# Performance work log

Hardware: AMD Instinct MI355X
Metric: run time of the kernel (lower is better)

The kernel has to match this reference:

```python
import jax, jax.numpy as jnp
import numpy as np

D_MODEL = 512
N_HEADS = 8
HEAD_DIM = D_MODEL // N_HEADS
B, L, S = 4, 2048, 2048


def setup_inputs() -> dict:
    key = jax.random.key(0)
    ks = jax.random.split(key, 16)
    std = 1.0 / np.sqrt(D_MODEL)
    inp = {
        'queries': jax.random.normal(ks[0], (B, L, D_MODEL), jnp.float32),
        'keys': jax.random.normal(ks[1], (B, S, D_MODEL), jnp.float32),
        'values': jax.random.normal(ks[2], (B, S, D_MODEL), jnp.float32),
        'tau': jax.random.uniform(ks[3], (B,), jnp.float32, 0.5, 1.5),
        'delta': jax.random.normal(ks[4], (B,), jnp.float32) * 0.1,
        'Wq': jax.random.normal(ks[5], (D_MODEL, D_MODEL), jnp.float32) * std,
        'bq': jnp.zeros((D_MODEL,), jnp.float32),
        'Wk': jax.random.normal(ks[6], (D_MODEL, D_MODEL), jnp.float32) * std,
        'bk': jnp.zeros((D_MODEL,), jnp.float32),
        'Wv': jax.random.normal(ks[7], (D_MODEL, D_MODEL), jnp.float32) * std,
        'bv': jnp.zeros((D_MODEL,), jnp.float32),
        'Wo': jax.random.normal(ks[8], (D_MODEL, D_MODEL), jnp.float32) * std,
        'bo': jnp.zeros((D_MODEL,), jnp.float32),
    }
    return inp


def reference(queries, keys, values, tau, delta, Wq, bq, Wk, bk, Wv, bv, Wo, bo):
    Bq, Lq, _ = queries.shape
    Sk = keys.shape[1]
    H, E = N_HEADS, HEAD_DIM
    # projections -> [B, L, H, E]
    q = (queries @ Wq + bq).reshape(Bq, Lq, H, E)
    k = (keys @ Wk + bk).reshape(Bq, Sk, H, E)
    v = (values @ Wv + bv).reshape(Bq, Sk, H, E)
    scale = 1.0 / jnp.sqrt(jnp.float32(E))
    # scores: [B, H, L, S]
    scores = jnp.einsum('blhe,bshe->bhls', q, k)
    scores = scores * tau[:, None, None, None] + delta[:, None, None, None]
    A = jax.nn.softmax(scale * scores, axis=-1)  # dropout is identity in eval
    out = jnp.einsum('bhls,bshd->blhd', A, v).reshape(Bq, Lq, H * E)
    return out @ Wo + bo
```

## Files before the change

kernel.cpp:

```cpp
#include <hip/hip_runtime.h>
#include <stdint.h>

#define NB 4
#define LQ 2048
#define DM 512
#define NH 8
#define EH 64
#define MT (NB*LQ)
#define QBLK 128

typedef __attribute__((ext_vector_type(4)))  float f32x4;
typedef __attribute__((ext_vector_type(8)))  __bf16 bf16x8;
typedef __attribute__((ext_vector_type(8)))  unsigned short u16x8;
typedef __attribute__((ext_vector_type(4)))  short s16x4;
typedef __attribute__((ext_vector_type(4)))  float float4_t;
typedef __attribute__((ext_vector_type(2)))  unsigned int u32x2;
typedef __attribute__((ext_vector_type(4)))  unsigned int u32x4;

static __device__ __forceinline__ unsigned short f2bf(float f) {
  unsigned int u = __builtin_bit_cast(unsigned int, f);
  u += 0x7fffu + ((u >> 16) & 1u);
  return (unsigned short)(u >> 16);
}

static __device__ __forceinline__ float bf2f(unsigned short h) {
  unsigned int u = ((unsigned int)h) << 16;
  return __builtin_bit_cast(float, u);
}

static __device__ __forceinline__ void gload16(const void* g, void* l) {
  __builtin_amdgcn_global_load_lds(
      (__attribute__((address_space(1))) unsigned int*)(g),
      (__attribute__((address_space(3))) unsigned int*)(l), 16, 0, 0);
}

static __device__ __forceinline__ unsigned int cvt_pk_bf16(float lo, float hi) {
  unsigned int r;
  asm("v_cvt_pk_bf16_f32 %0, %1, %2" : "=v"(r) : "v"(lo), "v"(hi));
  return r;
}

static __device__ __forceinline__ f32x4 mfma16(s16x4 a, s16x4 b, f32x4 c) {
#if defined(__HIP_DEVICE_COMPILE__)
#if __has_builtin(__builtin_amdgcn_mfma_f32_16x16x16bf16_1k)
  return __builtin_amdgcn_mfma_f32_16x16x16bf16_1k(a, b, c, 0, 0, 0);
#else
  f32x4 d;
  asm volatile("v_mfma_f32_16x16x16_bf16 %0, %1, %2, %3"
               : "=v"(d) : "v"(a), "v"(b), "0"(c));
  return d;
#endif
#else
  (void)a; (void)b;
  return c;
#endif
}

extern "C" __global__ __launch_bounds__(256) void k_cast_wt(
    const float* __restrict__ wq, const float* __restrict__ wk,
    const float* __restrict__ wv, const float* __restrict__ wo,
    unsigned short* __restrict__ wt) {
  __shared__ float tile[64][65];
  int z = blockIdx.z;
  const float* w = (z==0)?wq : (z==1)?wk : (z==2)?wv : wo;
  unsigned short* dst = wt + (size_t)z * DM * DM;
  int kb = blockIdx.y * 64, nb = blockIdx.x * 64;
  int t = threadIdx.x;
  int r = t >> 2, c0 = (t & 3) * 16;
  #pragma unroll
  for (int i = 0; i < 16; i += 4) {
    float4_t v4 = *(const float4_t*)(w + (size_t)(kb + r) * DM + nb + c0 + i);
    tile[r][c0+i]   = v4[0]; tile[r][c0+i+1] = v4[1];
    tile[r][c0+i+2] = v4[2]; tile[r][c0+i+3] = v4[3];
  }
  __syncthreads();
  u16x8 o0, o1;
  #pragma unroll
  for (int i = 0; i < 8; ++i) o0[i] = f2bf(tile[c0+i][r]);
  #pragma unroll
  for (int i = 0; i < 8; ++i) o1[i] = f2bf(tile[c0+8+i][r]);
  *(u16x8*)(dst + (size_t)(nb + r) * DM + kb + c0)     = o0;
  *(u16x8*)(dst + (size_t)(nb + r) * DM + kb + c0 + 8) = o1;
}

extern "C" __global__ __launch_bounds__(256) void k_gemm_qkv(
    const float* __restrict__ qin, const float* __restrict__ kin,
    const float* __restrict__ vin, const unsigned short* __restrict__ WT,
    const float* __restrict__ bq, const float* __restrict__ bk,
    const float* __restrict__ bv, const float* __restrict__ tau,
    unsigned short* __restrict__ out) {
  int bid = blockIdx.x;
  int wgid = (bid & 7) * 96 + (bid >> 3);
  int n0 = (wgid & 3) * 128;
  int p = wgid >> 2;
  int z = p % 3;
  int m0 = (p / 3) * 128;

  const float* Af = (z==0)?qin : (z==1)?kin : vin;
  const unsigned short* Bt = WT + (size_t)z * DM * DM;
  const float* bias = (z==0)?bq : (z==1)?bk : bv;
  unsigned short* dst = out + (size_t)z * MT * DM;

  __shared__ unsigned short As[2][128][32];
  __shared__ unsigned short Bs[2][128][32];

  float qsc = (z == 0) ? tau[m0 >> 11] * 0.18033688011112042f : 1.0f;
  int t = threadIdx.x;
  int lane = t & 63;
  int w = t >> 6;
  int wr = w >> 1, wc = w & 1;
  int g = lane >> 4, r15 = lane & 15;

  int ar = t >> 1, ah = t & 1;
  int as = (ar >> 1) & 3;
  int dlo = ((ah*2)     ^ as) * 8;
  int dhi = ((ah*2 + 1) ^ as) * 8;

  float4_t a0, a1, a2, a3;
  auto loadA = [&](int kt) {
    const float* src = Af + (size_t)(m0 + ar)*DM + kt*32 + ah*16;
    a0 = *(const float4_t*)(src);
    a1 = *(const float4_t*)(src + 4);
    a2 = *(const float4_t*)(src + 8);
    a3 = *(const float4_t*)(src + 12);
  };
  auto writeA = [&](int bb) {
    u32x4 lo, hi;
    lo[0] = cvt_pk_bf16(a0[0], a0[1]); lo[1] = cvt_pk_bf16(a0[2], a0[3]);
    lo[2] = cvt_pk_bf16(a1[0], a1[1]); lo[3] = cvt_pk_bf16(a1[2], a1[3]);
    hi[0] = cvt_pk_bf16(a2[0], a2[1]); hi[1] = cvt_pk_bf16(a2[2], a2[3]);
    hi[2] = cvt_pk_bf16(a3[0], a3[1]); hi[3] = cvt_pk_bf16(a3[2], a3[3]);
    *(u32x4*)(&As[bb][ar][dlo]) = lo;
    *(u32x4*)(&As[bb][ar][dhi]) = hi;
  };
  auto stageB = [&](int bb, int kt) {
    int k0 = kt * 32;
    int sblk = (t & 3) ^ ((t >> 3) & 3);
    #pragma unroll
    for (int j=0;j<2;j++) {
      int o = t*16 + j*4096;
      int row = o >> 6;
      gload16(Bt + (size_t)(n0+row)*DM + k0 + sblk*8, (char*)(&Bs[bb][0][0]) + o);
    }
  };

  f32x4 acc[4][4];
  #pragma unroll
  for (int i=0;i<4;i++)
    #pragma unroll
    for (int j=0;j<4;j++)
      #pragma unroll
      for (int e=0;e<4;e++) acc[i][j][e] = 0.f;

  loadA(0);
  writeA(0);
  stageB(0, 0);
  __syncthreads();
  int buf = 0;
  for (int kt = 0; kt < DM/32; ++kt) {
    bool pre = (kt + 1 < DM/32);
    if (pre) { loadA(kt + 1); stageB(buf ^ 1, kt + 1); }
    bf16x8 af[4], bfr[4];
    #pragma unroll
    for (int mi=0;mi<4;mi++) {
      int row = wr*64 + mi*16 + r15;
      int blk = g ^ ((row >> 1) & 3);
      af[mi] = *(const bf16x8*)(&As[buf][row][blk*8]);
    }
    #pragma unroll
    for (int ni=0;ni<4;ni++) {
      int row = wc*64 + ni*16 + r15;
      int blk = g ^ ((row >> 1) & 3);
      bfr[ni] = *(const bf16x8*)(&Bs[buf][row][blk*8]);
    }
    #pragma unroll
    for (int mi=0;mi<4;mi++)
      #pragma unroll
      for (int ni=0;ni<4;ni++)
        acc[mi][ni] = __builtin_amdgcn_mfma_f32_16x16x32_bf16(af[mi], bfr[ni], acc[mi][ni], 0, 0, 0);
    if (pre) writeA(buf ^ 1);
    __syncthreads();
    buf ^= 1;
  }
  #pragma unroll
  for (int ni=0;ni<4;ni++) {
    int n = n0 + wc*64 + ni*16 + r15;
    float bia = bias[n];
    int h = n >> 6, e = n & 63;
    #pragma unroll
    for (int mi=0;mi<4;mi++) {
      #pragma unroll
      for (int rg=0;rg<4;rg++) {
        int m = m0 + wr*64 + mi*16 + g*4 + rg;
        int b = m >> 11, s = m & 2047;
        dst[((size_t)((b*NH + h)*LQ + s))*EH + e] = f2bf((acc[mi][ni][rg] + bia) * qsc);
      }
    }
  }
}

extern "C" __global__ __launch_bounds__(256) void k_vt(
    const unsigned short* __restrict__ qkv, unsigned short* __restrict__ vtg) {
  __shared__ unsigned short tile[64][65];
  int bh = blockIdx.y;
  int s0 = blockIdx.x * 64;
  const unsigned short* Vh = qkv + (size_t)2*MT*DM + (size_t)bh*LQ*EH;
  unsigned short* Ot = vtg + (size_t)bh*EH*LQ;
  int t = threadIdx.x;
  int r = t >> 2, c0 = (t & 3) * 16;
  u16x8 a = *(const u16x8*)(Vh + (size_t)(s0 + r)*EH + c0);
  u16x8 b = *(const u16x8*)(Vh + (size_t)(s0 + r)*EH + c0 + 8);
  #pragma unroll
  for (int i=0;i<8;i++) { tile[r][c0+i] = a[i]; tile[r][c0+8+i] = b[i]; }
  __syncthreads();
  int gg = t & 3;
  int er = t >> 2;
  int s2 = (er ^ (er >> 3)) & 3;
  #pragma unroll
  for (int blk = 0; blk < 2; ++blk) {
    u16x8 o;
    #pragma unroll
    for (int j = 0; j < 8; ++j) {
      int sp = blk*32 + (j >> 2)*16 + gg*4 + (j & 3);
      o[j] = tile[sp][er];
    }
    *(u16x8*)(Ot + (size_t)er*LQ + s0 + blk*32 + 8*(gg ^ s2)) = o;
  }
}

template<int NSPLIT>
__global__ __launch_bounds__(256, 4) void k_flash(
    const unsigned short* __restrict__ qkv, const unsigned short* __restrict__ vtg,
    unsigned short* __restrict__ aout,
    unsigned short* __restrict__ opart, float* __restrict__ lpart) {
  constexpr int SKV = LQ / NSPLIT;
  constexpr int NIT = SKV / 32;
  constexpr int CPX = (512 * NSPLIT) / 8;
  int bid = blockIdx.x;
  int wgid = (bid & 7) * CPX + (bid >> 3);
  int part = wgid % NSPLIT;
  int rest = wgid / NSPLIT;
  int qblk = rest & 15;
  int bh = rest >> 4;
  int batch = bh >> 3, h = bh & 7;

  const unsigned short* Qh  = qkv + (size_t)bh * LQ * EH + (size_t)qblk * QBLK * EH;
  const unsigned short* Kh  = qkv + (size_t)MT * DM + (size_t)bh * LQ * EH + (size_t)part * SKV * EH;
  const unsigned short* VTh = vtg + (size_t)bh * EH * LQ + (size_t)part * SKV;

  __shared__ unsigned short Ks[3][32][64];
  __shared__ unsigned short Vt[3][64][32];

  int t = threadIdx.x;
  int lane = t & 63;
  int wv = t >> 6;
  int q4 = lane & 15;
  int g  = lane >> 4;

  auto stage = [&](int bb, int it) {
    int o = t * 16;
    int krow = t >> 3;
    int sblk = (t & 7) ^ ((krow ^ (krow >> 3)) & 7);
    gload16(Kh + (size_t)(it*32 + krow)*EH + sblk*8, (char*)(&Ks[bb][0][0]) + o);
    gload16(VTh + (size_t)(t >> 2)*LQ + it*32 + (t & 3)*8, (char*)(&Vt[bb][0][0]) + o);
  };

  bf16x8 qf[2][2];
  #pragma unroll
  for (int qt=0;qt<2;qt++)
    #pragma unroll
    for (int st=0;st<2;st++)
      qf[qt][st] = *(const bf16x8*)(Qh + (size_t)(wv*32 + qt*16 + q4)*EH + st*32 + g*8);

  const f32x4 Z4 = {0.f, 0.f, 0.f, 0.f};
  f32x4 oacc[4][2];
  #pragma unroll
  for (int a=0;a<4;a++)
    #pragma unroll
    for (int b2=0;b2<2;b2++)
      #pragma unroll
      for (int e=0;e<4;e++) oacc[a][b2][e] = 0.f;
  float lsp[2] = {0.f, 0.f};

  stage(0, 0);
  if (NIT > 1) stage(1, 1);
  asm volatile("s_waitcnt vmcnt(0)" ::: "memory");
  __builtin_amdgcn_s_barrier();

  for (int it = 0; it < NIT; ++it) {
    int buf = it % 3;
    __builtin_amdgcn_s_barrier();
    if (it + 2 < NIT) stage((it + 2) % 3, it + 2);
    asm volatile("s_waitcnt vmcnt(4)" ::: "memory");
    __builtin_amdgcn_s_barrier();
    __builtin_amdgcn_sched_barrier(0);

    f32x4 sac[2][2];
    __builtin_amdgcn_s_setprio(1);
    #pragma unroll
    for (int kvt=0; kvt<2; ++kvt) {
      int row = kvt*16 + q4;
      int S = (row ^ (row >> 3)) & 7;
      bf16x8 kf0 = *(const bf16x8*)(&Ks[buf][row][(g ^ S)*8]);
      sac[kvt][0] = __builtin_amdgcn_mfma_f32_16x16x32_bf16(kf0, qf[0][0], Z4, 0,0,0);
      sac[kvt][1] = __builtin_amdgcn_mfma_f32_16x16x32_bf16(kf0, qf[1][0], Z4, 0,0,0);
    }
    #pragma unroll
    for (int kvt=0; kvt<2; ++kvt) {
      int row = kvt*16 + q4;
      int S = (row ^ (row >> 3)) & 7;
      bf16x8 kf1 = *(const bf16x8*)(&Ks[buf][row][((4 + g) ^ S)*8]);
      sac[kvt][0] = __builtin_amdgcn_mfma_f32_16x16x32_bf16(kf1, qf[0][1], sac[kvt][0], 0,0,0);
      sac[kvt][1] = __builtin_amdgcn_mfma_f32_16x16x32_bf16(kf1, qf[1][1], sac[kvt][1], 0,0,0);
    }
    __builtin_amdgcn_s_setprio(0);

    s16x4 pk[2][2];
    #pragma unroll
    for (int qt=0; qt<2; ++qt) {
      #pragma unroll
      for (int kvt=0; kvt<2; ++kvt) {
        float p0 = __builtin_amdgcn_exp2f(sac[kvt][qt][0]);
        float p1 = __builtin_amdgcn_exp2f(sac[kvt][qt][1]);
        float p2 = __builtin_amdgcn_exp2f(sac[kvt][qt][2]);
        float p3 = __builtin_amdgcn_exp2f(sac[kvt][qt][3]);
        lsp[qt] += (p0 + p1) + (p2 + p3);
        union { u32x2 u; s16x4 h; } pu;
        pu.u[0] = cvt_pk_bf16(p0, p1);
        pu.u[1] = cvt_pk_bf16(p2, p3);
        pk[qt][kvt] = pu.h;
      }
    }

    __builtin_amdgcn_s_setprio(1);
    #pragma unroll
    for (int et=0; et<4; ++et) {
      int row = et*16 + q4;
      int s2 = (row ^ (row >> 3)) & 3;
      union { u16x8 w; s16x4 h[2]; } vu;
      vu.w = *(const u16x8*)(&Vt[buf][row][(g ^ s2)*8]);
      oacc[et][0] = mfma16(vu.h[0], pk[0][0], oacc[et][0]);
      oacc[et][0] = mfma16(vu.h[1], pk[0][1], oacc[et][0]);
      oacc[et][1] = mfma16(vu.h[0], pk[1][0], oacc[et][1]);
      oacc[et][1] = mfma16(vu.h[1], pk[1][1], oacc[et][1]);
    }
    __builtin_amdgcn_s_setprio(0);
  }

  #pragma unroll
  for (int qt=0; qt<2; ++qt) {
    float s = lsp[qt];
    s += __shfl_xor(s, 16, 64);
    s += __shfl_xor(s, 32, 64);
    int q = qblk*QBLK + wv*32 + qt*16 + q4;
    if constexpr (NSPLIT == 1) {
      float inv = 1.f / s;
      unsigned short* rowp = aout + (size_t)(batch*LQ + q)*DM + h*EH;
      #pragma unroll
      for (int et=0; et<4; ++et) {
        #pragma unroll
        for (int rg=0; rg<4; rg+=2) {
          int e = et*16 + g*4 + rg;
          *(unsigned int*)(rowp + e) = cvt_pk_bf16(oacc[et][qt][rg] * inv, oacc[et][qt][rg+1] * inv);
        }
      }
    } else {
      size_t r = (size_t)bh * LQ + q;
      unsigned short* od = opart + ((size_t)r*NSPLIT + part) * 64;
      #pragma unroll
      for (int et=0; et<4; ++et) {
        u32x2 wpk;
        wpk[0] = cvt_pk_bf16(oacc[et][qt][0], oacc[et][qt][1]);
        wpk[1] = cvt_pk_bf16(oacc[et][qt][2], oacc[et][qt][3]);
        *(u32x2*)(od + et*16 + g*4) = wpk;
      }
      if (g == 0) lpart[r*NSPLIT + part] = s;
    }
  }
}

extern "C" __global__ __launch_bounds__(256) void k_red(
    const unsigned short* __restrict__ op, const float* __restrict__ lp,
    unsigned short* __restrict__ aout) {
  int t = threadIdx.x;
  int r = blockIdx.x * 16 + (t >> 4);
  int e0 = (t & 15) * 4;
  float acc0 = 0.f, acc1 = 0.f, acc2 = 0.f, acc3 = 0.f, ls = 0.f;
  #pragma unroll
  for (int qq = 0; qq < 4; ++qq) {
    u32x2 wv = *(const u32x2*)(op + ((size_t)r*4 + qq)*64 + e0);
    acc0 += bf2f((unsigned short)(wv[0] & 0xFFFF));
    acc1 += bf2f((unsigned short)(wv[0] >> 16));
    acc2 += bf2f((unsigned short)(wv[1] & 0xFFFF));
    acc3 += bf2f((unsigned short)(wv[1] >> 16));
    ls += lp[(size_t)r*4 + qq];
  }
  float inv = 1.f / ls;
  int bh = r >> 11, q = r & 2047, batch = bh >> 3, h = bh & 7;
  unsigned short* dst = aout + (size_t)(batch*LQ + q)*DM + h*EH + e0;
  u32x2 w;
  w[0] = cvt_pk_bf16(acc0 * inv, acc1 * inv);
  w[1] = cvt_pk_bf16(acc2 * inv, acc3 * inv);
  *(u32x2*)dst = w;
}

extern "C" __global__ __launch_bounds__(256) void k_gemm_out(
    const unsigned short* __restrict__ A, const unsigned short* __restrict__ WT,
    const float* __restrict__ bo, float* __restrict__ out) {
  const unsigned short* Bt = WT + (size_t)3 * DM * DM;

  __shared__ unsigned short As[2][128][32];
  __shared__ unsigned short Bs[2][128][32];

  int m0 = blockIdx.y * 128;
  int n0 = blockIdx.x * 128;
  int t = threadIdx.x;
  int lane = t & 63;
  int w = t >> 6;
  int wr = w >> 1, wc = w & 1;
  int g = lane >> 4, r15 = lane & 15;

  f32x4 acc[4][4];
  #pragma unroll
  for (int i=0;i<4;i++)
    #pragma unroll
    for (int j=0;j<4;j++)
      #pragma unroll
      for (int e=0;e<4;e++) acc[i][j][e] = 0.f;

  auto stage = [&](int bb, int kt) {
    int k0 = kt * 32;
    int sblk = (t & 3) ^ ((t >> 3) & 3);
    #pragma unroll
    for (int j=0;j<2;j++) {
      int o = t*16 + j*4096;
      int row = o >> 6;
      gload16(A  + (size_t)(m0+row)*DM + k0 + sblk*8, (char*)(&As[bb][0][0]) + o);
      gload16(Bt + (size_t)(n0+row)*DM + k0 + sblk*8, (char*)(&Bs[bb][0][0]) + o);
    }
  };

  stage(0, 0);
  __syncthreads();
  int buf = 0;
  for (int kt = 0; kt < DM/32; ++kt) {
    if (kt + 1 < DM/32) stage(buf ^ 1, kt + 1);
    bf16x8 af[4], bfr[4];
    #pragma unroll
    for (int mi=0;mi<4;mi++) {
      int row = wr*64 + mi*16 + r15;
      int blk = g ^ ((row >> 1) & 3);
      af[mi] = *(const bf16x8*)(&As[buf][row][blk*8]);
    }
    #pragma unroll
    for (int ni=0;ni<4;ni++) {
      int row = wc*64 + ni*16 + r15;
      int blk = g ^ ((row >> 1) & 3);
      bfr[ni] = *(const bf16x8*)(&Bs[buf][row][blk*8]);
    }
    #pragma unroll
    for (int mi=0;mi<4;mi++)
      #pragma unroll
      for (int ni=0;ni<4;ni++)
        acc[mi][ni] = __builtin_amdgcn_mfma_f32_16x16x32_bf16(af[mi], bfr[ni], acc[mi][ni], 0, 0, 0);
    __syncthreads();
    buf ^= 1;
  }
  #pragma unroll
  for (int ni=0;ni<4;ni++) {
    int n = n0 + wc*64 + ni*16 + r15;
    float bia = bo[n];
    #pragma unroll
    for (int mi=0;mi<4;mi++) {
      #pragma unroll
      for (int rg=0;rg<4;rg++) {
        int m = m0 + wr*64 + mi*16 + g*4 + rg;
        out[(size_t)m*DM + n] = acc[mi][ni][rg] + bia;
      }
    }
  }
}

extern "C" void kernel_launch(void* const* d_in, const int* in_sizes, int n_in,
                              void* d_out, int out_size, void* d_ws, size_t ws_size,
                              hipStream_t stream) {
  const float* queries = (const float*)d_in[0];
  const float* keys    = (const float*)d_in[1];
  const float* values  = (const float*)d_in[2];
  const float* tau     = (const float*)d_in[3];
  const float* Wq = (const float*)d_in[5];
  const float* bq = (const float*)d_in[6];
  const float* Wk = (const float*)d_in[7];
  const float* bk = (const float*)d_in[8];
  const float* Wv = (const float*)d_in[9];
  const float* bv = (const float*)d_in[10];
  const float* Wo = (const float*)d_in[11];
  const float* bo = (const float*)d_in[12];
  float* out = (float*)d_out;

  char* ws = (char*)d_ws;
  unsigned short* WT   = (unsigned short*)(ws);
  unsigned short* VTg  = (unsigned short*)(ws + (2u  << 20));
  unsigned short* AOut = (unsigned short*)(ws + (10u << 20));
  unsigned short* QKV  = (unsigned short*)(ws + (26u << 20));
  unsigned short* Opart= (unsigned short*)(ws + (50u << 20));
  float*          Lpart= (float*)(ws + (84u << 20));

  k_cast_wt <<<dim3(8, 8, 4), dim3(256), 0, stream>>>(Wq, Wk, Wv, Wo, WT);
  k_gemm_qkv<<<dim3(768), dim3(256), 0, stream>>>(queries, keys, values, WT,
                                                  bq, bk, bv, tau, QKV);
  k_vt      <<<dim3(32, 32), dim3(256), 0, stream>>>(QKV, VTg);

  if (ws_size >= ((size_t)85u << 20)) {
    k_flash<4><<<dim3(2048), dim3(256), 0, stream>>>(QKV, VTg, AOut, Opart, Lpart);
    k_red    <<<dim3(4096), dim3(256), 0, stream>>>(Opart, Lpart, AOut);
  } else {
    k_flash<1><<<dim3(512), dim3(256), 0, stream>>>(QKV, VTg, AOut, Opart, Lpart);
  }
  k_gemm_out<<<dim3(4, 64), dim3(256), 0, stream>>>(AOut, WT, bo, out);
}
```

Baseline: 108.3 us.

## Fuse V transpose into QKV GEMM and split-K reduce into output GEMM

The QKV projection epilogue now writes V directly in the transposed, swizzled layout that flash attention expects, so the separate transpose kernel goes away. The split-KV partial reduction and normalisation now happen while loading the A operand of the output projection GEMM, which removes the reduction kernel and the round trip of the attention output through memory. Flash attention also drops from a triple-buffered K/V pipeline with explicit waitcnt to a double buffer with __syncthreads, trading load/compute overlap for less LDS. The GEMM's A-tile loads become heavier, with four partials per element, and its global writes for V are strided across rows.

```diff
diff --git a/kernel.cpp b/kernel.cpp
--- a/kernel.cpp
+++ b/kernel.cpp
@@ -88,7 +88,7 @@
     const float* __restrict__ vin, const unsigned short* __restrict__ WT,
     const float* __restrict__ bq, const float* __restrict__ bk,
     const float* __restrict__ bv, const float* __restrict__ tau,
-    unsigned short* __restrict__ out) {
+    unsigned short* __restrict__ out, unsigned short* __restrict__ vtg) {
   int bid = blockIdx.x;
   int wgid = (bid & 7) * 96 + (bid >> 3);
   int n0 = (wgid & 3) * 128;
@@ -112,9 +112,9 @@
   int g = lane >> 4, r15 = lane & 15;
 
   int ar = t >> 1, ah = t & 1;
-  int as = (ar >> 1) & 3;
-  int dlo = ((ah*2)     ^ as) * 8;
-  int dhi = ((ah*2 + 1) ^ as) * 8;
+  int as_ = (ar >> 1) & 3;
+  int dlo = ((ah*2)     ^ as_) * 8;
+  int dhi = ((ah*2 + 1) ^ as_) * 8;
 
   float4_t a0, a1, a2, a3;
   auto loadA = [&](int kt) {
@@ -182,49 +182,42 @@
     __syncthreads();
     buf ^= 1;
   }
-  #pragma unroll
-  for (int ni=0;ni<4;ni++) {
-    int n = n0 + wc*64 + ni*16 + r15;
-    float bia = bias[n];
-    int h = n >> 6, e = n & 63;
-    #pragma unroll
-    for (int mi=0;mi<4;mi++) {
-      #pragma unroll
-      for (int rg=0;rg<4;rg++) {
-        int m = m0 + wr*64 + mi*16 + g*4 + rg;
+
+  if (z != 2) {
+    #pragma unroll
+    for (int ni=0;ni<4;ni++) {
+      int n = n0 + wc*64 + ni*16 + r15;
+      float bia = bias[n];
+      int h = n >> 6, e = n & 63;
+      #pragma unroll
+      for (int mi=0;mi<4;mi++) {
+        #pragma unroll
+        for (int rg=0;rg<4;rg++) {
+          int m = m0 + wr*64 + mi*16 + g*4 + rg;
+          int b = m >> 11, s = m & 2047;
+          dst[((size_t)((b*NH + h)*LQ + s))*EH + e] = f2bf((acc[mi][ni][rg] + bia) * qsc);
+        }
+      }
+    }
+  } else {
+    #pragma unroll
+    for (int ni=0;ni<4;ni++) {
+      int n = n0 + wc*64 + ni*16 + r15;
+      float bia = bias[n];
+      int h = n >> 6, e = n & 63;
+      int s2v = (e ^ (e >> 3)) & 3;
+      #pragma unroll
+      for (int mi=0;mi<4;mi++) {
+        int m = m0 + wr*64 + mi*16 + g*4;
         int b = m >> 11, s = m & 2047;
-        dst[((size_t)((b*NH + h)*LQ + s))*EH + e] = f2bf((acc[mi][ni][rg] + bia) * qsc);
+        int si = s & 31;
+        int pos = 8*(((si >> 2) & 3) ^ s2v) + 4*(si >> 4);
+        u32x2 wv;
+        wv[0] = cvt_pk_bf16(acc[mi][ni][0] + bia, acc[mi][ni][1] + bia);
+        wv[1] = cvt_pk_bf16(acc[mi][ni][2] + bia, acc[mi][ni][3] + bia);
+        *(u32x2*)(vtg + (size_t)(b*NH + h)*EH*LQ + (size_t)e*LQ + (s >> 5)*32 + pos) = wv;
       }
     }
-  }
-}
-
-extern "C" __global__ __launch_bounds__(256) void k_vt(
-    const unsigned short* __restrict__ qkv, unsigned short* __restrict__ vtg) {
-  __shared__ unsigned short tile[64][65];
-  int bh = blockIdx.y;
-  int s0 = blockIdx.x * 64;
-  const unsigned short* Vh = qkv + (size_t)2*MT*DM + (size_t)bh*LQ*EH;
-  unsigned short* Ot = vtg + (size_t)bh*EH*LQ;
-  int t = threadIdx.x;
-  int r = t >> 2, c0 = (t & 3) * 16;
-  u16x8 a = *(const u16x8*)(Vh + (size_t)(s0 + r)*EH + c0);
-  u16x8 b = *(const u16x8*)(Vh + (size_t)(s0 + r)*EH + c0 + 8);
-  #pragma unroll
-  for (int i=0;i<8;i++) { tile[r][c0+i] = a[i]; tile[r][c0+8+i] = b[i]; }
-  __syncthreads();
-  int gg = t & 3;
-  int er = t >> 2;
-  int s2 = (er ^ (er >> 3)) & 3;
-  #pragma unroll
-  for (int blk = 0; blk < 2; ++blk) {
-    u16x8 o;
-    #pragma unroll
-    for (int j = 0; j < 8; ++j) {
-      int sp = blk*32 + (j >> 2)*16 + gg*4 + (j & 3);
-      o[j] = tile[sp][er];
-    }
-    *(u16x8*)(Ot + (size_t)er*LQ + s0 + blk*32 + 8*(gg ^ s2)) = o;
   }
 }
 
@@ -248,8 +241,8 @@
   const unsigned short* Kh  = qkv + (size_t)MT * DM + (size_t)bh * LQ * EH + (size_t)part * SKV * EH;
   const unsigned short* VTh = vtg + (size_t)bh * EH * LQ + (size_t)part * SKV;
 
-  __shared__ unsigned short Ks[3][32][64];
-  __shared__ unsigned short Vt[3][64][32];
+  __shared__ unsigned short Ks[2][32][64];
+  __shared__ unsigned short Vt[2][64][32];
 
   int t = threadIdx.x;
   int lane = t & 63;
@@ -272,6 +265,8 @@
     for (int st=0;st<2;st++)
       qf[qt][st] = *(const bf16x8*)(Qh + (size_t)(wv*32 + qt*16 + q4)*EH + st*32 + g*8);
 
+  stage(0, 0);
+
   const f32x4 Z4 = {0.f, 0.f, 0.f, 0.f};
   f32x4 oacc[4][2];
   #pragma unroll
@@ -282,18 +277,10 @@
       for (int e=0;e<4;e++) oacc[a][b2][e] = 0.f;
   float lsp[2] = {0.f, 0.f};
 
-  stage(0, 0);
-  if (NIT > 1) stage(1, 1);
-  asm volatile("s_waitcnt vmcnt(0)" ::: "memory");
-  __builtin_amdgcn_s_barrier();
-
+  __syncthreads();
+  int buf = 0;
   for (int it = 0; it < NIT; ++it) {
-    int buf = it % 3;
-    __builtin_amdgcn_s_barrier();
-    if (it + 2 < NIT) stage((it + 2) % 3, it + 2);
-    asm volatile("s_waitcnt vmcnt(4)" ::: "memory");
-    __builtin_amdgcn_s_barrier();
-    __builtin_amdgcn_sched_barrier(0);
+    if (it + 1 < NIT) stage(buf ^ 1, it + 1);
 
     f32x4 sac[2][2];
     __builtin_amdgcn_s_setprio(1);
@@ -345,6 +332,9 @@
       oacc[et][1] = mfma16(vu.h[1], pk[1][1], oacc[et][1]);
     }
     __builtin_amdgcn_s_setprio(0);
+
+    __syncthreads();
+    buf ^= 1;
   }
 
   #pragma unroll
@@ -379,29 +369,128 @@
   }
 }
 
-extern "C" __global__ __launch_bounds__(256) void k_red(
+extern "C" __global__ __launch_bounds__(256) void k_gemm_out_f(
     const unsigned short* __restrict__ op, const float* __restrict__ lp,
-    unsigned short* __restrict__ aout) {
+    const unsigned short* __restrict__ WT, const float* __restrict__ bo,
+    float* __restrict__ out) {
+  const unsigned short* Bt = WT + (size_t)3 * DM * DM;
+
+  __shared__ unsigned short As[2][128][32];
+  __shared__ unsigned short Bs[2][128][32];
+
+  int bid = blockIdx.x;
+  int wgid = (bid & 7) * 32 + (bid >> 3);
+  int n0 = (wgid & 3) * 128;
+  int m0 = (wgid >> 2) * 128;
+
   int t = threadIdx.x;
-  int r = blockIdx.x * 16 + (t >> 4);
-  int e0 = (t & 15) * 4;
-  float acc0 = 0.f, acc1 = 0.f, acc2 = 0.f, acc3 = 0.f, ls = 0.f;
-  #pragma unroll
-  for (int qq = 0; qq < 4; ++qq) {
-    u32x2 wv = *(const u32x2*)(op + ((size_t)r*4 + qq)*64 + e0);
-    acc0 += bf2f((unsigned short)(wv[0] & 0xFFFF));
-    acc1 += bf2f((unsigned short)(wv[0] >> 16));
-    acc2 += bf2f((unsigned short)(wv[1] & 0xFFFF));
-    acc3 += bf2f((unsigned short)(wv[1] >> 16));
-    ls += lp[(size_t)r*4 + qq];
-  }
-  float inv = 1.f / ls;
-  int bh = r >> 11, q = r & 2047, batch = bh >> 3, h = bh & 7;
-  unsigned short* dst = aout + (size_t)(batch*LQ + q)*DM + h*EH + e0;
-  u32x2 w;
-  w[0] = cvt_pk_bf16(acc0 * inv, acc1 * inv);
-  w[1] = cvt_pk_bf16(acc2 * inv, acc3 * inv);
-  *(u32x2*)dst = w;
+  int lane = t & 63;
+  int w = t >> 6;
+  int wr = w >> 1, wc = w & 1;
+  int g = lane >> 4, r15 = lane & 15;
+
+  int ar = t >> 1, ah = t & 1;
+  int as_ = (ar >> 1) & 3;
+  int dlo = ((ah*2)     ^ as_) * 8;
+  int dhi = ((ah*2 + 1) ^ as_) * 8;
+  int m = m0 + ar;
+  int b = m >> 11, q = m & 2047;
+
+  float invh[8];
+  #pragma unroll
+  for (int hh=0; hh<8; ++hh) {
+    size_t r4 = (size_t)((b*NH + hh)*LQ + q) * 4;
+    invh[hh] = 1.f / (lp[r4] + lp[r4+1] + lp[r4+2] + lp[r4+3]);
+  }
+
+  u16x8 pa[4], pb[4];
+  auto loadA = [&](int kt) {
+    int hh = kt >> 1;
+    const unsigned short* src = op + (size_t)((b*NH + hh)*LQ + q) * 256 + (kt & 1)*32 + ah*16;
+    #pragma unroll
+    for (int p=0; p<4; ++p) {
+      pa[p] = *(const u16x8*)(src + p*64);
+      pb[p] = *(const u16x8*)(src + p*64 + 8);
+    }
+  };
+  auto writeA = [&](int bb, int kt) {
+    float inv = invh[kt >> 1];
+    float f0[8], f1[8];
+    #pragma unroll
+    for (int j=0;j<8;j++) {
+      f0[j] = ((bf2f(pa[0][j]) + bf2f(pa[1][j])) + (bf2f(pa[2][j]) + bf2f(pa[3][j]))) * inv;
+      f1[j] = ((bf2f(pb[0][j]) + bf2f(pb[1][j])) + (bf2f(pb[2][j]) + bf2f(pb[3][j]))) * inv;
+    }
+    u32x4 lo, hi;
+    #pragma unroll
+    for (int j=0;j<4;j++) lo[j] = cvt_pk_bf16(f0[2*j], f0[2*j+1]);
+    #pragma unroll
+    for (int j=0;j<4;j++) hi[j] = cvt_pk_bf16(f1[2*j], f1[2*j+1]);
+    *(u32x4*)(&As[bb][ar][dlo]) = lo;
+    *(u32x4*)(&As[bb][ar][dhi]) = hi;
+  };
+  auto stageB = [&](int bb, int kt) {
+    int k0 = kt * 32;
+    int sblk = (t & 3) ^ ((t >> 3) & 3);
+    #pragma unroll
+    for (int j=0;j<2;j++) {
+      int o = t*16 + j*4096;
+      int row = o >> 6;
+      gload16(Bt + (size_t)(n0+row)*DM + k0 + sblk*8, (char*)(&Bs[bb][0][0]) + o);
+    }
+  };
+
+  f32x4 acc[4][4];
+  #pragma unroll
+  for (int i=0;i<4;i++)
+    #pragma unroll
+    for (int j=0;j<4;j++)
+      #pragma unroll
+      for (int e=0;e<4;e++) acc[i][j][e] = 0.f;
+
+  loadA(0);
+  writeA(0, 0);
+  stageB(0, 0);
+  __syncthreads();
+  int buf = 0;
+  for (int kt = 0; kt < DM/32; ++kt) {
+    bool pre = (kt + 1 < DM/32);
+    if (pre) { loadA(kt + 1); stageB(buf ^ 1, kt + 1); }
+    bf16x8 af[4], bfr[4];
+    #pragma unroll
+    for (int mi=0;mi<4;mi++) {
+      int row = wr*64 + mi*16 + r15;
+      int blk = g ^ ((row >> 1) & 3);
+      af[mi] = *(const bf16x8*)(&As[buf][row][blk*8]);
+    }
+    #pragma unroll
+    for (int ni=0;ni<4;ni++) {
+      int row = wc*64 + ni*16 + r15;
+      int blk = g ^ ((row >> 1) & 3);
+      bfr[ni] = *(const bf16x8*)(&Bs[buf][row][blk*8]);
+    }
+    #pragma unroll
+    for (int mi=0;mi<4;mi++)
+      #pragma unroll
+      for (int ni=0;ni<4;ni++)
+        acc[mi][ni] = __builtin_amdgcn_mfma_f32_16x16x32_bf16(af[mi], bfr[ni], acc[mi][ni], 0, 0, 0);
+    if (pre) writeA(buf ^ 1, kt + 1);
+    __syncthreads();
+    buf ^= 1;
+  }
+  #pragma unroll
+  for (int ni=0;ni<4;ni++) {
+    int n = n0 + wc*64 + ni*16 + r15;
+    float bia = bo[n];
+    #pragma unroll
+    for (int mi=0;mi<4;mi++) {
+      #pragma unroll
+      for (int rg=0;rg<4;rg++) {
+        int mm = m0 + wr*64 + mi*16 + g*4 + rg;
+        out[(size_t)mm*DM + n] = acc[mi][ni][rg] + bia;
+      }
+    }
+  }
 }
 
 extern "C" __global__ __launch_bounds__(256) void k_gemm_out(
@@ -501,21 +590,20 @@
   char* ws = (char*)d_ws;
   unsigned short* WT   = (unsigned short*)(ws);
   unsigned short* VTg  = (unsigned short*)(ws + (2u  << 20));
-  unsigned short* AOut = (unsigned short*)(ws + (10u << 20));
-  unsigned short* QKV  = (unsigned short*)(ws + (26u << 20));
-  unsigned short* Opart= (unsigned short*)(ws + (50u << 20));
-  float*          Lpart= (float*)(ws + (84u << 20));
+  unsigned short* QKV  = (unsigned short*)(ws + (10u << 20));
+  unsigned short* Opart= (unsigned short*)(ws + (34u << 20));
+  float*          Lpart= (float*)(ws + (68u << 20));
+  unsigned short* AOutF= (unsigned short*)(ws + (34u << 20));
 
   k_cast_wt <<<dim3(8, 8, 4), dim3(256), 0, stream>>>(Wq, Wk, Wv, Wo, WT);
   k_gemm_qkv<<<dim3(768), dim3(256), 0, stream>>>(queries, keys, values, WT,
-                                                  bq, bk, bv, tau, QKV);
-  k_vt      <<<dim3(32, 32), dim3(256), 0, stream>>>(QKV, VTg);
-
-  if (ws_size >= ((size_t)85u << 20)) {
-    k_flash<4><<<dim3(2048), dim3(256), 0, stream>>>(QKV, VTg, AOut, Opart, Lpart);
-    k_red    <<<dim3(4096), dim3(256), 0, stream>>>(Opart, Lpart, AOut);
+                                                  bq, bk, bv, tau, QKV, VTg);
+
+  if (ws_size >= ((size_t)70u << 20)) {
+    k_flash<4>  <<<dim3(2048), dim3(256), 0, stream>>>(QKV, VTg, AOutF, Opart, Lpart);
+    k_gemm_out_f<<<dim3(256), dim3(256), 0, stream>>>(Opart, Lpart, WT, bo, out);
   } else {
-    k_flash<1><<<dim3(512), dim3(256), 0, stream>>>(QKV, VTg, AOut, Opart, Lpart);
-  }
-  k_gemm_out<<<dim3(4, 64), dim3(256), 0, stream>>>(AOut, WT, bo, out);
-}
+    k_flash<1>  <<<dim3(512), dim3(256), 0, stream>>>(QKV, VTg, AOutF, Opart, Lpart);
+    k_gemm_out  <<<dim3(4, 64), dim3(256), 0, stream>>>(AOutF, WT, bo, out);
+  }
+}
```

After: 120.9 us. 1.12x slower.

## Fuse V transpose into QKV GEMM epilogue and simplify flash pipeline to double buffer

Applied to the files above, without the earlier changes.

The V projection epilogue now writes the swizzled transposed V layout directly, which removes the separate k_vt kernel and its global read/write pass. The flash attention kernel's triple-buffered staging with explicit vmcnt waits becomes a double-buffered loop with __syncthreads, lowering LDS use. The workspace layout is compacted. The transposed stores are narrower and less coalesced, and the shallower pipeline may hide load latency less well.

```diff
diff --git a/kernel.cpp b/kernel.cpp
--- a/kernel.cpp
+++ b/kernel.cpp
@@ -88,7 +88,7 @@
     const float* __restrict__ vin, const unsigned short* __restrict__ WT,
     const float* __restrict__ bq, const float* __restrict__ bk,
     const float* __restrict__ bv, const float* __restrict__ tau,
-    unsigned short* __restrict__ out) {
+    unsigned short* __restrict__ out, unsigned short* __restrict__ vtg) {
   int bid = blockIdx.x;
   int wgid = (bid & 7) * 96 + (bid >> 3);
   int n0 = (wgid & 3) * 128;
@@ -112,9 +112,9 @@
   int g = lane >> 4, r15 = lane & 15;
 
   int ar = t >> 1, ah = t & 1;
-  int as = (ar >> 1) & 3;
-  int dlo = ((ah*2)     ^ as) * 8;
-  int dhi = ((ah*2 + 1) ^ as) * 8;
+  int as_ = (ar >> 1) & 3;
+  int dlo = ((ah*2)     ^ as_) * 8;
+  int dhi = ((ah*2 + 1) ^ as_) * 8;
 
   float4_t a0, a1, a2, a3;
   auto loadA = [&](int kt) {
@@ -182,49 +182,42 @@
     __syncthreads();
     buf ^= 1;
   }
-  #pragma unroll
-  for (int ni=0;ni<4;ni++) {
-    int n = n0 + wc*64 + ni*16 + r15;
-    float bia = bias[n];
-    int h = n >> 6, e = n & 63;
-    #pragma unroll
-    for (int mi=0;mi<4;mi++) {
-      #pragma unroll
-      for (int rg=0;rg<4;rg++) {
-        int m = m0 + wr*64 + mi*16 + g*4 + rg;
+
+  if (z != 2) {
+    #pragma unroll
+    for (int ni=0;ni<4;ni++) {
+      int n = n0 + wc*64 + ni*16 + r15;
+      float bia = bias[n];
+      int h = n >> 6, e = n & 63;
+      #pragma unroll
+      for (int mi=0;mi<4;mi++) {
+        #pragma unroll
+        for (int rg=0;rg<4;rg++) {
+          int m = m0 + wr*64 + mi*16 + g*4 + rg;
+          int b = m >> 11, s = m & 2047;
+          dst[((size_t)((b*NH + h)*LQ + s))*EH + e] = f2bf((acc[mi][ni][rg] + bia) * qsc);
+        }
+      }
+    }
+  } else {
+    #pragma unroll
+    for (int ni=0;ni<4;ni++) {
+      int n = n0 + wc*64 + ni*16 + r15;
+      float bia = bias[n];
+      int h = n >> 6, e = n & 63;
+      int s2v = (e ^ (e >> 3)) & 3;
+      #pragma unroll
+      for (int mi=0;mi<4;mi++) {
+        int m = m0 + wr*64 + mi*16 + g*4;
         int b = m >> 11, s = m & 2047;
-        dst[((size_t)((b*NH + h)*LQ + s))*EH + e] = f2bf((acc[mi][ni][rg] + bia) * qsc);
+        int si = s & 31;
+        int pos = 8*(((si >> 2) & 3) ^ s2v) + 4*(si >> 4);
+        u32x2 wv;
+        wv[0] = cvt_pk_bf16(acc[mi][ni][0] + bia, acc[mi][ni][1] + bia);
+        wv[1] = cvt_pk_bf16(acc[mi][ni][2] + bia, acc[mi][ni][3] + bia);
+        *(u32x2*)(vtg + (size_t)(b*NH + h)*EH*LQ + (size_t)e*LQ + (s >> 5)*32 + pos) = wv;
       }
     }
-  }
-}
-
-extern "C" __global__ __launch_bounds__(256) void k_vt(
-    const unsigned short* __restrict__ qkv, unsigned short* __restrict__ vtg) {
-  __shared__ unsigned short tile[64][65];
-  int bh = blockIdx.y;
-  int s0 = blockIdx.x * 64;
-  const unsigned short* Vh = qkv + (size_t)2*MT*DM + (size_t)bh*LQ*EH;
-  unsigned short* Ot = vtg + (size_t)bh*EH*LQ;
-  int t = threadIdx.x;
-  int r = t >> 2, c0 = (t & 3) * 16;
-  u16x8 a = *(const u16x8*)(Vh + (size_t)(s0 + r)*EH + c0);
-  u16x8 b = *(const u16x8*)(Vh + (size_t)(s0 + r)*EH + c0 + 8);
-  #pragma unroll
-  for (int i=0;i<8;i++) { tile[r][c0+i] = a[i]; tile[r][c0+8+i] = b[i]; }
-  __syncthreads();
-  int gg = t & 3;
-  int er = t >> 2;
-  int s2 = (er ^ (er >> 3)) & 3;
-  #pragma unroll
-  for (int blk = 0; blk < 2; ++blk) {
-    u16x8 o;
-    #pragma unroll
-    for (int j = 0; j < 8; ++j) {
-      int sp = blk*32 + (j >> 2)*16 + gg*4 + (j & 3);
-      o[j] = tile[sp][er];
-    }
-    *(u16x8*)(Ot + (size_t)er*LQ + s0 + blk*32 + 8*(gg ^ s2)) = o;
   }
 }
 
@@ -248,8 +241,8 @@
   const unsigned short* Kh  = qkv + (size_t)MT * DM + (size_t)bh * LQ * EH + (size_t)part * SKV * EH;
   const unsigned short* VTh = vtg + (size_t)bh * EH * LQ + (size_t)part * SKV;
 
-  __shared__ unsigned short Ks[3][32][64];
-  __shared__ unsigned short Vt[3][64][32];
+  __shared__ unsigned short Ks[2][32][64];
+  __shared__ unsigned short Vt[2][64][32];
 
   int t = threadIdx.x;
   int lane = t & 63;
@@ -272,6 +265,8 @@
     for (int st=0;st<2;st++)
       qf[qt][st] = *(const bf16x8*)(Qh + (size_t)(wv*32 + qt*16 + q4)*EH + st*32 + g*8);
 
+  stage(0, 0);
+
   const f32x4 Z4 = {0.f, 0.f, 0.f, 0.f};
   f32x4 oacc[4][2];
   #pragma unroll
@@ -282,18 +277,10 @@
       for (int e=0;e<4;e++) oacc[a][b2][e] = 0.f;
   float lsp[2] = {0.f, 0.f};
 
-  stage(0, 0);
-  if (NIT > 1) stage(1, 1);
-  asm volatile("s_waitcnt vmcnt(0)" ::: "memory");
-  __builtin_amdgcn_s_barrier();
-
+  __syncthreads();
+  int buf = 0;
   for (int it = 0; it < NIT; ++it) {
-    int buf = it % 3;
-    __builtin_amdgcn_s_barrier();
-    if (it + 2 < NIT) stage((it + 2) % 3, it + 2);
-    asm volatile("s_waitcnt vmcnt(4)" ::: "memory");
-    __builtin_amdgcn_s_barrier();
-    __builtin_amdgcn_sched_barrier(0);
+    if (it + 1 < NIT) stage(buf ^ 1, it + 1);
 
     f32x4 sac[2][2];
     __builtin_amdgcn_s_setprio(1);
@@ -345,6 +332,9 @@
       oacc[et][1] = mfma16(vu.h[1], pk[1][1], oacc[et][1]);
     }
     __builtin_amdgcn_s_setprio(0);
+
+    __syncthreads();
+    buf ^= 1;
   }
 
   #pragma unroll
@@ -501,19 +491,18 @@
   char* ws = (char*)d_ws;
   unsigned short* WT   = (unsigned short*)(ws);
   unsigned short* VTg  = (unsigned short*)(ws + (2u  << 20));
-  unsigned short* AOut = (unsigned short*)(ws + (10u << 20));
-  unsigned short* QKV  = (unsigned short*)(ws + (26u << 20));
-  unsigned short* Opart= (unsigned short*)(ws + (50u << 20));
-  float*          Lpart= (float*)(ws + (84u << 20));
+  unsigned short* QKV  = (unsigned short*)(ws + (10u << 20));
+  unsigned short* Opart= (unsigned short*)(ws + (34u << 20));
+  float*          Lpart= (float*)(ws + (68u << 20));
+  unsigned short* AOut = (unsigned short*)(ws + (69u << 20));
 
   k_cast_wt <<<dim3(8, 8, 4), dim3(256), 0, stream>>>(Wq, Wk, Wv, Wo, WT);
   k_gemm_qkv<<<dim3(768), dim3(256), 0, stream>>>(queries, keys, values, WT,
-                                                  bq, bk, bv, tau, QKV);
-  k_vt      <<<dim3(32, 32), dim3(256), 0, stream>>>(QKV, VTg);
-
-  if (ws_size >= ((size_t)85u << 20)) {
+                                                  bq, bk, bv, tau, QKV, VTg);
+
+  if (ws_size >= ((size_t)78u << 20)) {
     k_flash<4><<<dim3(2048), dim3(256), 0, stream>>>(QKV, VTg, AOut, Opart, Lpart);
-    k_red    <<<dim3(4096), dim3(256), 0, stream>>>(Opart, Lpart, AOut);
+    k_red     <<<dim3(4096), dim3(256), 0, stream>>>(Opart, Lpart, AOut);
   } else {
     k_flash<1><<<dim3(512), dim3(256), 0, stream>>>(QKV, VTg, AOut, Opart, Lpart);
   }
```

After: 112.3 us. 1.04x slower.
